# Optimization experiments

Hardware: AMD Instinct MI355X
Metric: run time of the kernel (lower is better)

The kernel has to match this reference:

```python
import jax, jax.numpy as jnp
import numpy as np


def _chain_edges(n):
    # bidirectional chain edges + self loops (PyG GATConv add_self_loops=True default)
    src = np.concatenate([np.arange(n - 1), np.arange(1, n), np.arange(n)])
    dst = np.concatenate([np.arange(1, n), np.arange(n - 1), np.arange(n)])
    return jnp.asarray(src), jnp.asarray(dst)


def _gat(x, W, a_src, a_dst, bias, src, dst, n, heads, ch, concat):
    # x: [B, n, Fin]; PyG GATConv v1 math (lin has no bias, bias added post-agg)
    B = x.shape[0]
    xh = (x @ W).reshape(B, n, heads, ch)  # [B,n,h,c]
    es = jnp.einsum('bnhc,hc->bnh', xh, a_src)
    ed = jnp.einsum('bnhc,hc->bnh', xh, a_dst)
    e = jax.nn.leaky_relu(es[:, src] + ed[:, dst], 0.2)  # [B,E,h]
    e = jnp.moveaxis(e, 1, 0)                            # [E,B,h]
    m = jax.ops.segment_max(e, dst, num_segments=n)      # scatter-softmax over incoming edges
    w = jnp.exp(e - m[dst])
    denom = jax.ops.segment_sum(w, dst, num_segments=n)
    alpha = w / denom[dst]                               # [E,B,h]
    msgs = alpha[..., None] * jnp.moveaxis(xh[:, src], 1, 0)  # [E,B,h,c]
    out = jnp.moveaxis(jax.ops.segment_sum(msgs, dst, num_segments=n), 0, 1)  # [B,n,h,c]
    out = out.reshape(B, n, heads * ch) if concat else out.mean(axis=2)
    return out + bias


def _mlp(x, w1, b1, w2, b2, w3, b3):
    h = jax.nn.leaky_relu(x @ w1 + b1, 0.01)
    h = jax.nn.leaky_relu(h @ w2 + b2, 0.01)
    return h @ w3 + b3


def setup_inputs() -> dict:
    key = jax.random.key(0)
    ks = jax.random.split(key, 21)
    B, n, d_state, hid, da = 2048, 50, 64, 128, 4
    r = lambda k, shp, s: (jax.random.normal(k, shp, dtype=jnp.float32) * s)
    return {
        'state': r(ks[0], (B, n, d_state), 1.0),
        'W1': r(ks[1], (d_state, 2 * hid), 0.1), 'att_src1': r(ks[2], (2, hid), 0.1),
        'att_dst1': r(ks[3], (2, hid), 0.1), 'b1': r(ks[4], (2 * hid,), 0.02),
        'W2': r(ks[5], (2 * hid, hid), 0.1), 'att_src2': r(ks[6], (1, hid), 0.1),
        'att_dst2': r(ks[7], (1, hid), 0.1), 'b2': r(ks[8], (hid,), 0.02),
        'aw1': r(ks[9], (hid, 128), 0.1), 'ab1': r(ks[10], (128,), 0.02),
        'aw2': r(ks[11], (128, 128), 0.1), 'ab2': r(ks[12], (128,), 0.02),
        'aw3': r(ks[13], (128, da), 0.1), 'ab3': r(ks[14], (da,), 0.02),
        'vw1': r(ks[15], (hid, 128), 0.1), 'vb1': r(ks[16], (128,), 0.02),
        'vw2': r(ks[17], (128, 128), 0.1), 'vb2': r(ks[18], (128,), 0.02),
        'vw3': r(ks[19], (128, 1), 0.1), 'vb3': r(ks[20], (1,), 0.02),
    }


def reference(state, W1, att_src1, att_dst1, b1, W2, att_src2, att_dst2, b2,
              aw1, ab1, aw2, ab2, aw3, ab3, vw1, vb1, vw2, vb2, vw3, vb3):
    B, n, _ = state.shape
    src, dst = _chain_edges(n)
    x = jax.nn.gelu(_gat(state, W1, att_src1, att_dst1, b1, src, dst, n, 2, 128, True), approximate=False)
    x = jax.nn.gelu(_gat(x, W2, att_src2, att_dst2, b2, src, dst, n, 1, 128, False), approximate=False)
    graph_emb = x.mean(axis=1)                      # global_mean_pool over chain nodes
    value = _mlp(graph_emb, vw1, vb1, vw2, vb2, vw3, vb3)   # [B,1]
    mean = _mlp(x, aw1, ab1, aw2, ab2, aw3, ab3).reshape(B, -1)  # [B, n*d_action]
    return mean, value
```

## Files before the change

kernel.cpp:

```cpp
#include <hip/hip_runtime.h>

#define DI __device__ __forceinline__

typedef unsigned int uint32;
typedef unsigned short u16;
typedef __attribute__((ext_vector_type(8))) short s8v;
typedef __attribute__((ext_vector_type(4))) float f4v;

DI float lrelu(float x, float s){ return x > 0.f ? x : s*x; }
DI float fastrcp(float x){ float r; asm("v_rcp_f32 %0, %1" : "=v"(r) : "v"(x)); return r; }
DI u16 f2bu(float f){ uint32 u = __float_as_uint(f); return (u16)((u + 0x7FFFu + ((u>>16)&1u)) >> 16); }
DI float b16f(u16 u){ return __uint_as_float(((uint32)u)<<16); }

DI float gelu_f(float x){
  const float z = fabsf(x) * 0.70710678118654752f;
  const float t = fastrcp(1.f + 0.3275911f*z);
  float p = 1.061405429f;
  p = p*t - 1.453152027f;
  p = p*t + 1.421413741f;
  p = p*t - 0.284496736f;
  p = p*t + 0.254829592f;
  p = p*t;
  const float e = __expf(-z*z);
  float er = 1.f - p*e;
  er = copysignf(er, x);
  return 0.5f*x*(1.f + er);
}

DI f4v mfma16(s8v a, s8v b, f4v c){
  return __builtin_amdgcn_mfma_f32_16x16x32_bf16(a, b, c, 0, 0, 0);
}

constexpr int NNODE = 50;
constexpr int NT = 512;
constexpr int SCS = 134;

constexpr int WS1  = 0;
constexpr int WS2  = 18432;
constexpr int WSA1 = 55296;
constexpr int WSA2 = 71680;
constexpr int WSA3 = 88064;
constexpr int WSTOT= 90112;

__global__ __launch_bounds__(256)
void ac_prep(const float* __restrict__ w1, const float* __restrict__ as1, const float* __restrict__ ad1,
             const float* __restrict__ w2, const float* __restrict__ as2, const float* __restrict__ ad2,
             const float* __restrict__ aw1, const float* __restrict__ aw2, const float* __restrict__ aw3,
             u16* __restrict__ ws)
{
  const int T1 = 2*144*64, T2 = 144*256, T3 = 128*128;
  for (int t = blockIdx.x*blockDim.x + threadIdx.x; t < WSTOT; t += gridDim.x*blockDim.x){
    float v; int o;
    if (t < T1){
      int h = t / 9216, r = t - h*9216, n = r>>6, k = r&63;
      if (n < 128) v = w1[k*256 + h*128 + n];
      else if (n < 130){
        const float* av = ((n==129) ? ad1 : as1) + h*128;
        const float* wr = w1 + k*256 + h*128;
        float s = 0.f;
        for (int c=0;c<128;++c) s += wr[c]*av[c];
        v = s;
      } else v = 0.f;
      o = WS1 + h*9216 + n*64 + k;
    } else if (t < T1+T2){
      int j = t - T1, n = j>>8, k = j&255;
      if (n < 128) v = w2[k*128 + n];
      else if (n < 130){
        const float* av = (n==129) ? ad2 : as2;
        const float* wr = w2 + k*128;
        float s = 0.f;
        for (int c=0;c<128;++c) s += wr[c]*av[c];
        v = s;
      } else v = 0.f;
      o = WS2 + n*256 + k;
    } else if (t < T1+T2+T3){
      int j = t - T1 - T2, n = j>>7, k = j&127;
      v = aw1[k*128 + n];
      o = WSA1 + n*128 + k;
    } else if (t < T1+T2+2*T3){
      int j = t - T1 - T2 - T3, n = j>>7, k = j&127;
      v = aw2[k*128 + n];
      o = WSA2 + n*128 + k;
    } else {
      int j = t - T1 - T2 - 2*T3, m = j>>7, k = j&127;
      v = (m < 4) ? aw3[k*4 + m] : 0.f;
      o = WSA3 + m*128 + k;
    }
    ws[o] = f2bu(v);
  }
}


__global__ __launch_bounds__(NT)
void ac_main(const float* __restrict__ state,
             const float* __restrict__ b1, const float* __restrict__ b2,
             const float* __restrict__ ab1, const float* __restrict__ ab2,
             const float* __restrict__ ab3,
             const float* __restrict__ vw1, const float* __restrict__ vb1,
             const float* __restrict__ vw2, const float* __restrict__ vb2,
             const float* __restrict__ vw3, const float* __restrict__ vb3,
             const u16* __restrict__ ws,
             float* __restrict__ out_mean, float* __restrict__ out_val)
{
  __shared__ __align__(16) float sm[13228];
  u16*   pAb  = (u16*)sm;
  u16*   pAs  = (u16*)sm;
  float* gebP = sm + 3200;
  float* vh1  = sm + 3712;
  float* sc   = sm + 6400;
  u16*   pAb2 = (u16*)(sm + 6400);
  float* geb  = sm + 13100;

  const int tid = threadIdx.x, b = blockIdx.x;
  const int wid = tid>>6, l15 = tid&15, g = (tid>>4)&3;

  {
    const float4* xb4 = (const float4*)(state + (size_t)b * (NNODE*64));
    for (int t = tid; t < 800; t += NT){
      float4 v = xb4[t];
      int i = t>>4, k0 = (t&15)*4;
      ushort4 u;
      u.x = f2bu(v.x); u.y = f2bu(v.y); u.z = f2bu(v.z); u.w = f2bu(v.w);
      *(ushort4*)(pAs + i*64 + (k0 ^ ((i&7)<<3))) = u;
    }
  }
  __syncthreads();

  s8v aS[4][2];
  #pragma unroll
  for (int mt=0;mt<4;++mt)
    #pragma unroll
    for (int ks=0;ks<2;++ks){
      int row = mt*16 + l15, c = ks*32 + g*8;
      aS[mt][ks] = *(const s8v*)(pAs + row*64 + (c ^ ((row&7)<<3)));
    }

  for (int h=0; h<2; ++h){
    for (int nt = wid; nt < 9; nt += 8){
      f4v acc[4];
      #pragma unroll
      for (int mt=0;mt<4;++mt) acc[mt] = (f4v){0.f,0.f,0.f,0.f};
      #pragma unroll
      for (int ks=0;ks<2;++ks){
        s8v bf = *(const s8v*)(ws + WS1 + h*9216 + (nt*16 + l15)*64 + ks*32 + g*8);
        #pragma unroll
        for (int mt=0;mt<4;++mt) acc[mt] = mfma16(aS[mt][ks], bf, acc[mt]);
      }
      const int col = nt*16 + l15;
      if (col < 130){
        #pragma unroll
        for (int mt=0;mt<4;++mt){
          #pragma unroll
          for (int r=0;r<4;++r){
            const int row = mt*16 + g*4 + r;
            if (mt < 3 || row < NNODE) sc[row*SCS + col] = acc[mt][r];
          }
        }
      }
    }
    __syncthreads();

    {
      const int i = tid & 63;
      if (i < NNODE){
        const float edi = sc[i*SCS + 129];
        const float eS = __expf(lrelu(sc[i*SCS + 128] + edi, 0.2f));
        const float eL = (i > 0)       ? __expf(lrelu(sc[(i-1)*SCS + 128] + edi, 0.2f)) : 0.f;
        const float eR = (i < NNODE-1) ? __expf(lrelu(sc[(i+1)*SCS + 128] + edi, 0.2f)) : 0.f;
        const float rs = fastrcp(eL + eS + eR);
        sc[i*SCS + 130] = eL*rs;
        sc[i*SCS + 131] = eS*rs;
        sc[i*SCS + 132] = eR*rs;
      }
    }
    {
      const int q = tid>>7, j = tid&127, jj = h*128 + j;
      const int i0 = q*13, i1 = (i0+13 < NNODE) ? i0+13 : NNODE;
      const float bj = b1[jj];
      float pv  = (i0 > 0) ? sc[(i0-1)*SCS + j] : 0.f;
      float cur = sc[i0*SCS + j];
      #pragma unroll 4
      for (int i = i0; i < i1; ++i){
        const float nx = (i < NNODE-1) ? sc[(i+1)*SCS + j] : 0.f;
        const float wL = sc[i*SCS + 130], wS = sc[i*SCS + 131], wR = sc[i*SCS + 132];
        const float v = gelu_f(wL*pv + wS*cur + wR*nx + bj);
        pAb[i*256 + (jj ^ ((i&7)<<3))] = f2bu(v);
        pv = cur; cur = nx;
      }
    }
    __syncthreads();
  }

  for (int nt = wid; nt < 9; nt += 8){
    f4v acc[4];
    #pragma unroll
    for (int mt=0;mt<4;++mt) acc[mt] = (f4v){0.f,0.f,0.f,0.f};
    #pragma unroll
    for (int ks=0;ks<8;++ks){
      s8v bf = *(const s8v*)(ws + WS2 + (nt*16 + l15)*256 + ks*32 + g*8);
      #pragma unroll
      for (int mt=0;mt<4;++mt){
        const int row = mt*16 + l15, c = ks*32 + g*8;
        s8v a = *(const s8v*)(pAb + row*256 + (c ^ ((row&7)<<3)));
        acc[mt] = mfma16(a, bf, acc[mt]);
      }
    }
    const int col = nt*16 + l15;
    if (col < 130){
      #pragma unroll
      for (int mt=0;mt<4;++mt){
        #pragma unroll
        for (int r=0;r<4;++r){
          const int row = mt*16 + g*4 + r;
          if (mt < 3 || row < NNODE) sc[row*SCS + col] = acc[mt][r];
        }
      }
    }
  }
  __syncthreads();

  {
    const int i = tid & 63;
    if (i < NNODE){
      const float edi = sc[i*SCS + 129];
      const float eS = __expf(lrelu(sc[i*SCS + 128] + edi, 0.2f));
      const float eL = (i > 0)       ? __expf(lrelu(sc[(i-1)*SCS + 128] + edi, 0.2f)) : 0.f;
      const float eR = (i < NNODE-1) ? __expf(lrelu(sc[(i+1)*SCS + 128] + edi, 0.2f)) : 0.f;
      const float rs = fastrcp(eL + eS + eR);
      sc[i*SCS + 130] = eL*rs;
      sc[i*SCS + 131] = eS*rs;
      sc[i*SCS + 132] = eR*rs;
    }
  }
  {
    const int q = tid>>7, j = tid&127;
    const int i0 = q*13, i1 = (i0+13 < NNODE) ? i0+13 : NNODE;
    const float bj = b2[j];
    float ps = 0.f;
    float pv  = (i0 > 0) ? sc[(i0-1)*SCS + j] : 0.f;
    float cur = sc[i0*SCS + j];
    #pragma unroll 4
    for (int i = i0; i < i1; ++i){
      const float nx = (i < NNODE-1) ? sc[(i+1)*SCS + j] : 0.f;
      const float wL = sc[i*SCS + 130], wS = sc[i*SCS + 131], wR = sc[i*SCS + 132];
      const float v = gelu_f(wL*pv + wS*cur + wR*nx + bj);
      pAb[i*128 + (j ^ ((i&7)<<3))] = f2bu(v);
      ps += v;
      pv = cur; cur = nx;
    }
    gebP[q*128 + j] = ps;
  }
  __syncthreads();

  {
    const int nt = wid;
    f4v acc[4];
    #pragma unroll
    for (int mt=0;mt<4;++mt) acc[mt] = (f4v){0.f,0.f,0.f,0.f};
    #pragma unroll
    for (int ks=0;ks<4;++ks){
      s8v bf = *(const s8v*)(ws + WSA1 + (nt*16 + l15)*128 + ks*32 + g*8);
      #pragma unroll
      for (int mt=0;mt<4;++mt){
        const int row = mt*16 + l15, c = ks*32 + g*8;
        s8v a = *(const s8v*)(pAb + row*128 + (c ^ ((row&7)<<3)));
        acc[mt] = mfma16(a, bf, acc[mt]);
      }
    }
    const int col = nt*16 + l15;
    const float bj = ab1[col];
    #pragma unroll
    for (int mt=0;mt<4;++mt){
      #pragma unroll
      for (int r=0;r<4;++r){
        const int row = mt*16 + g*4 + r;
        if (mt < 3 || row < NNODE){
          const float v = lrelu(acc[mt][r] + bj, 0.01f);
          pAb2[row*128 + (col ^ ((row&7)<<3))] = f2bu(v);
        }
      }
    }
    if (tid < 128)
      geb[tid] = (gebP[tid] + gebP[128+tid] + gebP[256+tid] + gebP[384+tid]) * 0.02f;
  }
  __syncthreads();

  {
    const int nt = wid;
    f4v acc[4];
    #pragma unroll
    for (int mt=0;mt<4;++mt) acc[mt] = (f4v){0.f,0.f,0.f,0.f};
    #pragma unroll
    for (int ks=0;ks<4;++ks){
      s8v bf = *(const s8v*)(ws + WSA2 + (nt*16 + l15)*128 + ks*32 + g*8);
      #pragma unroll
      for (int mt=0;mt<4;++mt){
        const int row = mt*16 + l15, c = ks*32 + g*8;
        s8v a = *(const s8v*)(pAb2 + row*128 + (c ^ ((row&7)<<3)));
        acc[mt] = mfma16(a, bf, acc[mt]);
      }
    }
    const int col = nt*16 + l15;
    const float bj = ab2[col];
    #pragma unroll
    for (int mt=0;mt<4;++mt){
      #pragma unroll
      for (int r=0;r<4;++r){
        const int row = mt*16 + g*4 + r;
        if (mt < 3 || row < NNODE){
          const float v = lrelu(acc[mt][r] + bj, 0.01f);
          pAb[row*128 + (col ^ ((row&7)<<3))] = f2bu(v);
        }
      }
    }
  }
  __syncthreads();

  if (wid < 4){
    const int mt = wid;
    f4v acc = (f4v){0.f,0.f,0.f,0.f};
    #pragma unroll
    for (int ks=0;ks<4;++ks){
      s8v bf = *(const s8v*)(ws + WSA3 + l15*128 + ks*32 + g*8);
      const int row = mt*16 + l15, c = ks*32 + g*8;
      s8v a = *(const s8v*)(pAb + row*128 + (c ^ ((row&7)<<3)));
      acc = mfma16(a, bf, acc);
    }
    if (l15 < 4){
      const float bj = ab3[l15];
      #pragma unroll
      for (int r=0;r<4;++r){
        const int row = mt*16 + g*4 + r;
        if (row < NNODE) out_mean[(size_t)b*200 + row*4 + l15] = acc[r] + bj;
      }
    }
  } else if (wid == 4){
    const int j = tid & 63;
    float a0=0.f, a1=0.f;
    #pragma unroll 4
    for (int k=0;k<128;++k){
      const float gk = geb[k];
      a0 += gk*vw1[k*128 + j];
      a1 += gk*vw1[k*128 + j + 64];
    }
    vh1[j]      = lrelu(a0 + vb1[j],    0.01f);
    vh1[j + 64] = lrelu(a1 + vb1[j+64], 0.01f);
    asm volatile("s_waitcnt lgkmcnt(0)" ::: "memory");
    __builtin_amdgcn_sched_barrier(0);
    float c0=0.f, c1=0.f;
    #pragma unroll 4
    for (int k=0;k<128;++k){
      const float hk = vh1[k];
      c0 += hk*vw2[k*128 + j];
      c1 += hk*vw2[k*128 + j + 64];
    }
    const float va = lrelu(c0 + vb2[j],    0.01f);
    const float vb = lrelu(c1 + vb2[j+64], 0.01f);
    float p = va*vw3[j] + vb*vw3[j+64];
    #pragma unroll
    for (int off=32; off>0; off>>=1) p += __shfl_down(p, off);
    if (j == 0) out_val[b] = p + vb3[0];
  }
}

extern "C" void kernel_launch(void* const* d_in, const int* in_sizes, int n_in,
                              void* d_out, int out_size, void* d_ws, size_t ws_size,
                              hipStream_t stream)
{
  const float* state = (const float*)d_in[0];
  const float* w1    = (const float*)d_in[1];
  const float* as1   = (const float*)d_in[2];
  const float* ad1   = (const float*)d_in[3];
  const float* b1_   = (const float*)d_in[4];
  const float* w2    = (const float*)d_in[5];
  const float* as2   = (const float*)d_in[6];
  const float* ad2   = (const float*)d_in[7];
  const float* b2_   = (const float*)d_in[8];
  const float* aw1   = (const float*)d_in[9];
  const float* ab1   = (const float*)d_in[10];
  const float* aw2   = (const float*)d_in[11];
  const float* ab2   = (const float*)d_in[12];
  const float* aw3   = (const float*)d_in[13];
  const float* ab3   = (const float*)d_in[14];
  const float* vw1   = (const float*)d_in[15];
  const float* vb1   = (const float*)d_in[16];
  const float* vw2   = (const float*)d_in[17];
  const float* vb2   = (const float*)d_in[18];
  const float* vw3   = (const float*)d_in[19];
  const float* vb3   = (const float*)d_in[20];

  const int B = in_sizes[0] / (NNODE * 64);
  float* out_mean = (float*)d_out;
  float* out_val  = out_mean + (size_t)B * 200;
  u16* ws = (u16*)d_ws;

  ac_prep<<<128, 256, 0, stream>>>(w1, as1, ad1, w2, as2, ad2, aw1, aw2, aw3, ws);
  ac_main<<<B, NT, 0, stream>>>(state, b1_, b2_, ab1, ab2, ab3,
                                vw1, vb1, vw2, vb2, vw3, vb3,
                                ws, out_mean, out_val);
}
```

Measured before the change: 148.1 us.

## Split fused kernel into GAT, action-head and value-head kernels via workspace

Splits the monolithic per-graph kernel into three launches. The first runs both GAT layers per graph and writes the second-layer bf16 activations to workspace. The second runs the action MLP over 64-row tiles of all nodes so that each MFMA tile is fully occupied. The third computes mean pooling and the value MLP with one wave per graph. This trades an extra global round trip of the intermediate activations (about 26 MB) and extra launches for better tile utilisation and lower per-block shared memory and register use; the old fused path is kept as a fallback when the workspace is too small.

Result: slower. 151.7 us (+2.4%).

```diff
diff --git a/kernel.cpp b/kernel.cpp
--- a/kernel.cpp
+++ b/kernel.cpp
@@ -41,6 +41,7 @@
 constexpr int WSA2 = 71680;
 constexpr int WSA3 = 88064;
 constexpr int WSTOT= 90112;
+constexpr int X2OFF= 90112;
 
 __global__ __launch_bounds__(256)
 void ac_prep(const float* __restrict__ w1, const float* __restrict__ as1, const float* __restrict__ ad1,
@@ -90,6 +91,304 @@
   }
 }
 
+__global__ __launch_bounds__(NT)
+void ac_gat(const float* __restrict__ state,
+            const float* __restrict__ b1, const float* __restrict__ b2,
+            u16* __restrict__ ws)
+{
+  __shared__ __align__(16) float sm[13100];
+  u16*   pAb = (u16*)sm;
+  u16*   pAs = (u16*)sm;
+  float* sc  = sm + 6400;
+
+  const int tid = threadIdx.x, b = blockIdx.x;
+  const int wid = tid>>6, l15 = tid&15, g = (tid>>4)&3;
+
+  {
+    const float4* xb4 = (const float4*)(state + (size_t)b * (NNODE*64));
+    for (int t = tid; t < 800; t += NT){
+      float4 v = xb4[t];
+      int i = t>>4, k0 = (t&15)*4;
+      ushort4 u;
+      u.x = f2bu(v.x); u.y = f2bu(v.y); u.z = f2bu(v.z); u.w = f2bu(v.w);
+      *(ushort4*)(pAs + i*64 + (k0 ^ ((i&7)<<3))) = u;
+    }
+  }
+  __syncthreads();
+
+  s8v aS[4][2];
+  #pragma unroll
+  for (int mt=0;mt<4;++mt)
+    #pragma unroll
+    for (int ks=0;ks<2;++ks){
+      int row = mt*16 + l15, c = ks*32 + g*8;
+      aS[mt][ks] = *(const s8v*)(pAs + row*64 + (c ^ ((row&7)<<3)));
+    }
+
+  for (int h=0; h<2; ++h){
+    for (int nt = wid; nt < 9; nt += 8){
+      f4v acc[4];
+      #pragma unroll
+      for (int mt=0;mt<4;++mt) acc[mt] = (f4v){0.f,0.f,0.f,0.f};
+      #pragma unroll
+      for (int ks=0;ks<2;++ks){
+        s8v bf = *(const s8v*)(ws + WS1 + h*9216 + (nt*16 + l15)*64 + ks*32 + g*8);
+        #pragma unroll
+        for (int mt=0;mt<4;++mt) acc[mt] = mfma16(aS[mt][ks], bf, acc[mt]);
+      }
+      const int col = nt*16 + l15;
+      if (col < 130){
+        #pragma unroll
+        for (int mt=0;mt<4;++mt){
+          #pragma unroll
+          for (int r=0;r<4;++r){
+            const int row = mt*16 + g*4 + r;
+            if (mt < 3 || row < NNODE) sc[row*SCS + col] = acc[mt][r];
+          }
+        }
+      }
+    }
+    __syncthreads();
+
+    {
+      const int i = tid & 63;
+      if (i < NNODE){
+        const float edi = sc[i*SCS + 129];
+        const float eS = __expf(lrelu(sc[i*SCS + 128] + edi, 0.2f));
+        const float eL = (i > 0)       ? __expf(lrelu(sc[(i-1)*SCS + 128] + edi, 0.2f)) : 0.f;
+        const float eR = (i < NNODE-1) ? __expf(lrelu(sc[(i+1)*SCS + 128] + edi, 0.2f)) : 0.f;
+        const float rs = fastrcp(eL + eS + eR);
+        sc[i*SCS + 130] = eL*rs;
+        sc[i*SCS + 131] = eS*rs;
+        sc[i*SCS + 132] = eR*rs;
+      }
+    }
+    {
+      const int q = tid>>7, j = tid&127, jj = h*128 + j;
+      const int i0 = q*13, i1 = (i0+13 < NNODE) ? i0+13 : NNODE;
+      const float bj = b1[jj];
+      float pv  = (i0 > 0) ? sc[(i0-1)*SCS + j] : 0.f;
+      float cur = sc[i0*SCS + j];
+      #pragma unroll 4
+      for (int i = i0; i < i1; ++i){
+        const float nx = (i < NNODE-1) ? sc[(i+1)*SCS + j] : 0.f;
+        const float wL = sc[i*SCS + 130], wS = sc[i*SCS + 131], wR = sc[i*SCS + 132];
+        const float v = gelu_f(wL*pv + wS*cur + wR*nx + bj);
+        pAb[i*256 + (jj ^ ((i&7)<<3))] = f2bu(v);
+        pv = cur; cur = nx;
+      }
+    }
+    __syncthreads();
+  }
+
+  for (int nt = wid; nt < 9; nt += 8){
+    f4v acc[4];
+    #pragma unroll
+    for (int mt=0;mt<4;++mt) acc[mt] = (f4v){0.f,0.f,0.f,0.f};
+    #pragma unroll
+    for (int ks=0;ks<8;++ks){
+      s8v bf = *(const s8v*)(ws + WS2 + (nt*16 + l15)*256 + ks*32 + g*8);
+      #pragma unroll
+      for (int mt=0;mt<4;++mt){
+        const int row = mt*16 + l15, c = ks*32 + g*8;
+        s8v a = *(const s8v*)(pAb + row*256 + (c ^ ((row&7)<<3)));
+        acc[mt] = mfma16(a, bf, acc[mt]);
+      }
+    }
+    const int col = nt*16 + l15;
+    if (col < 130){
+      #pragma unroll
+      for (int mt=0;mt<4;++mt){
+        #pragma unroll
+        for (int r=0;r<4;++r){
+          const int row = mt*16 + g*4 + r;
+          if (mt < 3 || row < NNODE) sc[row*SCS + col] = acc[mt][r];
+        }
+      }
+    }
+  }
+  __syncthreads();
+
+  {
+    const int i = tid & 63;
+    if (i < NNODE){
+      const float edi = sc[i*SCS + 129];
+      const float eS = __expf(lrelu(sc[i*SCS + 128] + edi, 0.2f));
+      const float eL = (i > 0)       ? __expf(lrelu(sc[(i-1)*SCS + 128] + edi, 0.2f)) : 0.f;
+      const float eR = (i < NNODE-1) ? __expf(lrelu(sc[(i+1)*SCS + 128] + edi, 0.2f)) : 0.f;
+      const float rs = fastrcp(eL + eS + eR);
+      sc[i*SCS + 130] = eL*rs;
+      sc[i*SCS + 131] = eS*rs;
+      sc[i*SCS + 132] = eR*rs;
+    }
+  }
+  {
+    u16* x2g = ws + X2OFF + (size_t)b * (NNODE*128);
+    const int q = tid>>7, j = tid&127;
+    const int i0 = q*13, i1 = (i0+13 < NNODE) ? i0+13 : NNODE;
+    const float bj = b2[j];
+    float pv  = (i0 > 0) ? sc[(i0-1)*SCS + j] : 0.f;
+    float cur = sc[i0*SCS + j];
+    #pragma unroll 4
+    for (int i = i0; i < i1; ++i){
+      const float nx = (i < NNODE-1) ? sc[(i+1)*SCS + j] : 0.f;
+      const float wL = sc[i*SCS + 130], wS = sc[i*SCS + 131], wR = sc[i*SCS + 132];
+      const float v = gelu_f(wL*pv + wS*cur + wR*nx + bj);
+      x2g[i*128 + j] = f2bu(v);
+      pv = cur; cur = nx;
+    }
+  }
+}
+
+__global__ __launch_bounds__(NT)
+void ac_head(const u16* __restrict__ ws,
+             const float* __restrict__ ab1, const float* __restrict__ ab2,
+             const float* __restrict__ ab3, float* __restrict__ out_mean, int headM)
+{
+  __shared__ __align__(16) float sm[8192];
+  u16* xt = (u16*)sm;
+  u16* a4 = (u16*)(sm + 4096);
+
+  const int tid = threadIdx.x, bid = blockIdx.x;
+  const int wid = tid>>6, l15 = tid&15, g = (tid>>4)&3;
+
+  {
+    const int row = tid>>3, c0 = (tid&7)*16;
+    const int grow = bid*64 + row;
+    if (grow < headM){
+      const uint4* src = (const uint4*)(ws + X2OFF + (size_t)grow*128 + c0);
+      uint4 v0 = src[0], v1 = src[1];
+      *(uint4*)(xt + row*128 + ( c0      ^ ((row&7)<<3))) = v0;
+      *(uint4*)(xt + row*128 + ((c0 + 8) ^ ((row&7)<<3))) = v1;
+    }
+  }
+  __syncthreads();
+
+  {
+    const int nt = wid;
+    f4v acc[4];
+    #pragma unroll
+    for (int mt=0;mt<4;++mt) acc[mt] = (f4v){0.f,0.f,0.f,0.f};
+    #pragma unroll
+    for (int ks=0;ks<4;++ks){
+      s8v bf = *(const s8v*)(ws + WSA1 + (nt*16 + l15)*128 + ks*32 + g*8);
+      #pragma unroll
+      for (int mt=0;mt<4;++mt){
+        const int row = mt*16 + l15, c = ks*32 + g*8;
+        s8v a = *(const s8v*)(xt + row*128 + (c ^ ((row&7)<<3)));
+        acc[mt] = mfma16(a, bf, acc[mt]);
+      }
+    }
+    const int col = nt*16 + l15;
+    const float bj = ab1[col];
+    #pragma unroll
+    for (int mt=0;mt<4;++mt)
+      #pragma unroll
+      for (int r=0;r<4;++r){
+        const int row = mt*16 + g*4 + r;
+        a4[row*128 + (col ^ ((row&7)<<3))] = f2bu(lrelu(acc[mt][r] + bj, 0.01f));
+      }
+  }
+  __syncthreads();
+
+  {
+    const int nt = wid;
+    f4v acc[4];
+    #pragma unroll
+    for (int mt=0;mt<4;++mt) acc[mt] = (f4v){0.f,0.f,0.f,0.f};
+    #pragma unroll
+    for (int ks=0;ks<4;++ks){
+      s8v bf = *(const s8v*)(ws + WSA2 + (nt*16 + l15)*128 + ks*32 + g*8);
+      #pragma unroll
+      for (int mt=0;mt<4;++mt){
+        const int row = mt*16 + l15, c = ks*32 + g*8;
+        s8v a = *(const s8v*)(a4 + row*128 + (c ^ ((row&7)<<3)));
+        acc[mt] = mfma16(a, bf, acc[mt]);
+      }
+    }
+    const int col = nt*16 + l15;
+    const float bj = ab2[col];
+    #pragma unroll
+    for (int mt=0;mt<4;++mt)
+      #pragma unroll
+      for (int r=0;r<4;++r){
+        const int row = mt*16 + g*4 + r;
+        xt[row*128 + (col ^ ((row&7)<<3))] = f2bu(lrelu(acc[mt][r] + bj, 0.01f));
+      }
+  }
+  __syncthreads();
+
+  if (wid < 4){
+    const int mt = wid;
+    f4v acc = (f4v){0.f,0.f,0.f,0.f};
+    #pragma unroll
+    for (int ks=0;ks<4;++ks){
+      s8v bf = *(const s8v*)(ws + WSA3 + l15*128 + ks*32 + g*8);
+      const int row = mt*16 + l15, c = ks*32 + g*8;
+      s8v a = *(const s8v*)(xt + row*128 + (c ^ ((row&7)<<3)));
+      acc = mfma16(a, bf, acc);
+    }
+    if (l15 < 4){
+      const float bj = ab3[l15];
+      #pragma unroll
+      for (int r=0;r<4;++r){
+        const int grow = bid*64 + mt*16 + g*4 + r;
+        if (grow < headM) out_mean[(size_t)grow*4 + l15] = acc[r] + bj;
+      }
+    }
+  }
+}
+
+__global__ __launch_bounds__(NT)
+void ac_value(const u16* __restrict__ ws,
+              const float* __restrict__ vw1, const float* __restrict__ vb1,
+              const float* __restrict__ vw2, const float* __restrict__ vb2,
+              const float* __restrict__ vw3, const float* __restrict__ vb3,
+              float* __restrict__ out_val, int B)
+{
+  __shared__ float gs[8*128];
+  __shared__ float vs[8*128];
+  const int tid = threadIdx.x, wid = tid>>6, j = tid&63;
+  const int b = blockIdx.x*8 + wid;
+  if (b >= B) return;
+  const u16* xb = ws + X2OFF + (size_t)b * (NNODE*128);
+
+  float g0 = 0.f, g1 = 0.f;
+  for (int i=0;i<NNODE;++i){
+    g0 += b16f(xb[i*128 + j]);
+    g1 += b16f(xb[i*128 + 64 + j]);
+  }
+  gs[wid*128 + j]      = g0 * 0.02f;
+  gs[wid*128 + 64 + j] = g1 * 0.02f;
+  asm volatile("s_waitcnt lgkmcnt(0)" ::: "memory");
+  __builtin_amdgcn_sched_barrier(0);
+
+  float a0=0.f, a1=0.f;
+  #pragma unroll 4
+  for (int k=0;k<128;++k){
+    const float gk = gs[wid*128 + k];
+    a0 += gk*vw1[k*128 + j];
+    a1 += gk*vw1[k*128 + j + 64];
+  }
+  vs[wid*128 + j]      = lrelu(a0 + vb1[j],    0.01f);
+  vs[wid*128 + 64 + j] = lrelu(a1 + vb1[j+64], 0.01f);
+  asm volatile("s_waitcnt lgkmcnt(0)" ::: "memory");
+  __builtin_amdgcn_sched_barrier(0);
+
+  float c0=0.f, c1=0.f;
+  #pragma unroll 4
+  for (int k=0;k<128;++k){
+    const float hk = vs[wid*128 + k];
+    c0 += hk*vw2[k*128 + j];
+    c1 += hk*vw2[k*128 + j + 64];
+  }
+  const float va = lrelu(c0 + vb2[j],    0.01f);
+  const float vb = lrelu(c1 + vb2[j+64], 0.01f);
+  float p = va*vw3[j] + vb*vw3[j+64];
+  #pragma unroll
+  for (int off=32; off>0; off>>=1) p += __shfl_down(p, off);
+  if (j == 0) out_val[b] = p + vb3[0];
+}
 
 __global__ __launch_bounds__(NT)
 void ac_main(const float* __restrict__ state,
@@ -159,7 +458,6 @@
       }
     }
     __syncthreads();
-
     {
       const int i = tid & 63;
       if (i < NNODE){
@@ -378,8 +676,8 @@
   const float* b2_   = (const float*)d_in[8];
   const float* aw1   = (const float*)d_in[9];
   const float* ab1   = (const float*)d_in[10];
+  const float* ab2   = (const float*)d_in[12];
   const float* aw2   = (const float*)d_in[11];
-  const float* ab2   = (const float*)d_in[12];
   const float* aw3   = (const float*)d_in[13];
   const float* ab3   = (const float*)d_in[14];
   const float* vw1   = (const float*)d_in[15];
@@ -394,8 +692,18 @@
   float* out_val  = out_mean + (size_t)B * 200;
   u16* ws = (u16*)d_ws;
 
+  const size_t need = ((size_t)X2OFF + (size_t)B * NNODE * 128) * 2;
+
   ac_prep<<<128, 256, 0, stream>>>(w1, as1, ad1, w2, as2, ad2, aw1, aw2, aw3, ws);
-  ac_main<<<B, NT, 0, stream>>>(state, b1_, b2_, ab1, ab2, ab3,
-                                vw1, vb1, vw2, vb2, vw3, vb3,
-                                ws, out_mean, out_val);
+
+  if (ws_size >= need){
+    const int headM = B * NNODE;
+    ac_gat<<<B, NT, 0, stream>>>(state, b1_, b2_, ws);
+    ac_head<<<(headM + 63)/64, NT, 0, stream>>>(ws, ab1, ab2, ab3, out_mean, headM);
+    ac_value<<<(B + 7)/8, NT, 0, stream>>>(ws, vw1, vb1, vw2, vb2, vw3, vb3, out_val, B);
+  } else {
+    ac_main<<<B, NT, 0, stream>>>(state, b1_, b2_, ab1, ab2, ab3,
+                                  vw1, vb1, vw2, vb2, vw3, vb3,
+                                  ws, out_mean, out_val);
+  }
 }
```

## Merge both GAT layer-1 heads into a single GEMM and aggregation pass

Applied to the files above, without the earlier changes.

Instead of looping over the two attention heads, each with its own GEMM, softmax and aggregation stages and barriers, the layer-1 projection is computed for all 256 columns plus four attention-score columns in one pass. The prep kernel repacks the weights into a single 272-row block. The score scratch buffer is widened to hold both heads, and aggregation now uses 256 threads per half of the nodes. This removes two barriers and improves MFMA work distribution (17 tiles over 8 waves instead of 9 per head). It costs more shared memory, which may lower occupancy.

New measurement: 140.7 us, median of 2. 1.05x faster.

```diff
diff --git a/kernel.cpp b/kernel.cpp
--- a/kernel.cpp
+++ b/kernel.cpp
@@ -33,14 +33,14 @@
 
 constexpr int NNODE = 50;
 constexpr int NT = 512;
-constexpr int SCS = 134;
+constexpr int SCS = 266;
 
 constexpr int WS1  = 0;
-constexpr int WS2  = 18432;
-constexpr int WSA1 = 55296;
-constexpr int WSA2 = 71680;
-constexpr int WSA3 = 88064;
-constexpr int WSTOT= 90112;
+constexpr int WS2  = 17408;
+constexpr int WSA1 = 54272;
+constexpr int WSA2 = 70656;
+constexpr int WSA3 = 87040;
+constexpr int WSTOT= 89088;
 
 __global__ __launch_bounds__(256)
 void ac_prep(const float* __restrict__ w1, const float* __restrict__ as1, const float* __restrict__ ad1,
@@ -48,20 +48,21 @@
              const float* __restrict__ aw1, const float* __restrict__ aw2, const float* __restrict__ aw3,
              u16* __restrict__ ws)
 {
-  const int T1 = 2*144*64, T2 = 144*256, T3 = 128*128;
+  const int T1 = 272*64, T2 = 144*256, T3 = 128*128;
   for (int t = blockIdx.x*blockDim.x + threadIdx.x; t < WSTOT; t += gridDim.x*blockDim.x){
     float v; int o;
     if (t < T1){
-      int h = t / 9216, r = t - h*9216, n = r>>6, k = r&63;
-      if (n < 128) v = w1[k*256 + h*128 + n];
-      else if (n < 130){
-        const float* av = ((n==129) ? ad1 : as1) + h*128;
+      int n = t>>6, k = t&63;
+      if (n < 256) v = w1[k*256 + n];
+      else if (n < 260){
+        int sd = (n-256)>>1, h = (n-256)&1;
+        const float* av = (sd ? ad1 : as1) + h*128;
         const float* wr = w1 + k*256 + h*128;
         float s = 0.f;
         for (int c=0;c<128;++c) s += wr[c]*av[c];
         v = s;
       } else v = 0.f;
-      o = WS1 + h*9216 + n*64 + k;
+      o = WS1 + n*64 + k;
     } else if (t < T1+T2){
       int j = t - T1, n = j>>8, k = j&255;
       if (n < 128) v = w2[k*128 + n];
@@ -102,14 +103,14 @@
              const u16* __restrict__ ws,
              float* __restrict__ out_mean, float* __restrict__ out_val)
 {
-  __shared__ __align__(16) float sm[13228];
+  __shared__ __align__(16) float sm[19828];
   u16*   pAb  = (u16*)sm;
   u16*   pAs  = (u16*)sm;
   float* gebP = sm + 3200;
   float* vh1  = sm + 3712;
   float* sc   = sm + 6400;
   u16*   pAb2 = (u16*)(sm + 6400);
-  float* geb  = sm + 13100;
+  float* geb  = sm + 19700;
 
   const int tid = threadIdx.x, b = blockIdx.x;
   const int wid = tid>>6, l15 = tid&15, g = (tid>>4)&3;
@@ -135,61 +136,63 @@
       aS[mt][ks] = *(const s8v*)(pAs + row*64 + (c ^ ((row&7)<<3)));
     }
 
-  for (int h=0; h<2; ++h){
-    for (int nt = wid; nt < 9; nt += 8){
-      f4v acc[4];
-      #pragma unroll
-      for (int mt=0;mt<4;++mt) acc[mt] = (f4v){0.f,0.f,0.f,0.f};
-      #pragma unroll
-      for (int ks=0;ks<2;++ks){
-        s8v bf = *(const s8v*)(ws + WS1 + h*9216 + (nt*16 + l15)*64 + ks*32 + g*8);
+  for (int nt = wid; nt < 17; nt += 8){
+    f4v acc[4];
+    #pragma unroll
+    for (int mt=0;mt<4;++mt) acc[mt] = (f4v){0.f,0.f,0.f,0.f};
+    #pragma unroll
+    for (int ks=0;ks<2;++ks){
+      s8v bf = *(const s8v*)(ws + WS1 + (nt*16 + l15)*64 + ks*32 + g*8);
+      #pragma unroll
+      for (int mt=0;mt<4;++mt) acc[mt] = mfma16(aS[mt][ks], bf, acc[mt]);
+    }
+    const int col = nt*16 + l15;
+    if (col < 260){
+      #pragma unroll
+      for (int mt=0;mt<4;++mt){
         #pragma unroll
-        for (int mt=0;mt<4;++mt) acc[mt] = mfma16(aS[mt][ks], bf, acc[mt]);
-      }
-      const int col = nt*16 + l15;
-      if (col < 130){
-        #pragma unroll
-        for (int mt=0;mt<4;++mt){
-          #pragma unroll
-          for (int r=0;r<4;++r){
-            const int row = mt*16 + g*4 + r;
-            if (mt < 3 || row < NNODE) sc[row*SCS + col] = acc[mt][r];
-          }
+        for (int r=0;r<4;++r){
+          const int row = mt*16 + g*4 + r;
+          if (mt < 3 || row < NNODE) sc[row*SCS + col] = acc[mt][r];
         }
       }
     }
-    __syncthreads();
-
-    {
-      const int i = tid & 63;
-      if (i < NNODE){
-        const float edi = sc[i*SCS + 129];
-        const float eS = __expf(lrelu(sc[i*SCS + 128] + edi, 0.2f));
-        const float eL = (i > 0)       ? __expf(lrelu(sc[(i-1)*SCS + 128] + edi, 0.2f)) : 0.f;
-        const float eR = (i < NNODE-1) ? __expf(lrelu(sc[(i+1)*SCS + 128] + edi, 0.2f)) : 0.f;
+  }
+  __syncthreads();
+
+  {
+    const int i = tid & 63;
+    if (i < NNODE){
+      #pragma unroll
+      for (int h=0;h<2;++h){
+        const float edi = sc[i*SCS + 258 + h];
+        const float eS = __expf(lrelu(sc[i*SCS + 256 + h] + edi, 0.2f));
+        const float eL = (i > 0)       ? __expf(lrelu(sc[(i-1)*SCS + 256 + h] + edi, 0.2f)) : 0.f;
+        const float eR = (i < NNODE-1) ? __expf(lrelu(sc[(i+1)*SCS + 256 + h] + edi, 0.2f)) : 0.f;
         const float rs = fastrcp(eL + eS + eR);
-        sc[i*SCS + 130] = eL*rs;
-        sc[i*SCS + 131] = eS*rs;
-        sc[i*SCS + 132] = eR*rs;
-      }
-    }
-    {
-      const int q = tid>>7, j = tid&127, jj = h*128 + j;
-      const int i0 = q*13, i1 = (i0+13 < NNODE) ? i0+13 : NNODE;
-      const float bj = b1[jj];
-      float pv  = (i0 > 0) ? sc[(i0-1)*SCS + j] : 0.f;
-      float cur = sc[i0*SCS + j];
-      #pragma unroll 4
-      for (int i = i0; i < i1; ++i){
-        const float nx = (i < NNODE-1) ? sc[(i+1)*SCS + j] : 0.f;
-        const float wL = sc[i*SCS + 130], wS = sc[i*SCS + 131], wR = sc[i*SCS + 132];
-        const float v = gelu_f(wL*pv + wS*cur + wR*nx + bj);
-        pAb[i*256 + (jj ^ ((i&7)<<3))] = f2bu(v);
-        pv = cur; cur = nx;
-      }
-    }
-    __syncthreads();
-  }
+        sc[i*SCS + 260 + h*3    ] = eL*rs;
+        sc[i*SCS + 260 + h*3 + 1] = eS*rs;
+        sc[i*SCS + 260 + h*3 + 2] = eR*rs;
+      }
+    }
+  }
+  {
+    const int q = tid>>8, j = tid&255, h = j>>7;
+    const int i0 = q*25, i1 = i0 + 25;
+    const float bj = b1[j];
+    const int wc = 260 + h*3;
+    float pv  = (i0 > 0) ? sc[(i0-1)*SCS + j] : 0.f;
+    float cur = sc[i0*SCS + j];
+    #pragma unroll 5
+    for (int i = i0; i < i1; ++i){
+      const float nx = (i < NNODE-1) ? sc[(i+1)*SCS + j] : 0.f;
+      const float wL = sc[i*SCS + wc], wS = sc[i*SCS + wc + 1], wR = sc[i*SCS + wc + 2];
+      const float v = gelu_f(wL*pv + wS*cur + wR*nx + bj);
+      pAb[i*256 + (j ^ ((i&7)<<3))] = f2bu(v);
+      pv = cur; cur = nx;
+    }
+  }
+  __syncthreads();
 
   for (int nt = wid; nt < 9; nt += 8){
     f4v acc[4];
```
